# Kernel optimization log

Hardware: AMD Instinct MI355X
Metric: run time of the kernel (lower is better)

Reference implementation:

```python
import jax, jax.numpy as jnp
import numpy as np

N_NODES = 2048
N_EDGES = 16384
D_FEAT = 4  # 2*D_FEAT = 8 qubit angles per edge

# TTN circuit gate sequence: ('ry', wire, theta_idx) or ('cx', control, target)
OPS = [("ry",1,0),("ry",2,1),("cx",1,2),
       ("ry",5,2),("ry",6,3),("cx",6,5),
       ("ry",0,4),("ry",1,5),("cx",0,1),
       ("ry",2,6),("ry",3,7),("cx",3,2),
       ("ry",4,8),("ry",5,9),("cx",4,5),
       ("ry",6,10),("ry",7,11),("cx",7,6),
       ("ry",2,12),("ry",5,13),("cx",2,5),
       ("ry",1,14),("ry",2,15),("cx",1,2),
       ("ry",5,16),("ry",6,17),("cx",6,5),
       ("ry",2,18),("ry",5,19),("cx",2,5),
       ("ry",5,20)]

def setup_inputs() -> dict:
    key = jax.random.key(0)
    k1, k2, k3, k4 = jax.random.split(key, 4)
    X = jax.random.normal(k1, (N_NODES, D_FEAT), dtype=jnp.float32)
    Ri = jax.random.normal(k2, (N_NODES, N_EDGES), dtype=jnp.float32)
    Ro = jax.random.normal(k3, (N_NODES, N_EDGES), dtype=jnp.float32)
    theta = jax.random.uniform(k4, (21,), dtype=jnp.float32) * (4.0 * np.pi)
    return {"X": X, "Ri": Ri, "Ro": Ro, "theta": theta}

def _ry(state, w, th):
    # state: [B, 2,2,2,2,2,2,2,2]; apply RY(th) on wire w (real rotation)
    c = jnp.cos(0.5 * th)
    s = jnp.sin(0.5 * th)
    a0 = jnp.take(state, 0, axis=w + 1)
    a1 = jnp.take(state, 1, axis=w + 1)
    return jnp.stack([c * a0 - s * a1, s * a0 + c * a1], axis=w + 1)

def _cnot(state, c, t):
    s0 = jnp.take(state, 0, axis=c + 1)  # control=0 branch: unchanged
    s1 = jnp.take(state, 1, axis=c + 1)  # control=1 branch: flip target
    t_ax = t + 1 if t < c else t  # axis shift after removing control axis
    s1 = jnp.flip(s1, axis=t_ax)
    return jnp.stack([s0, s1], axis=c + 1)

def _circuit(angles, theta):
    # angles: [B, 8] per-edge RY encoding angles; all gates real -> real statevector
    B = angles.shape[0]
    half = 0.5 * angles
    amps = jnp.stack([jnp.cos(half), jnp.sin(half)], axis=-1)  # [B, 8, 2], RY(a)|0>
    state = amps[:, 0, :]  # [B, 2]
    for q in range(1, 8):  # product state build-up -> [B, 2^8]
        state = state[..., None] * amps[:, q, :].reshape((B,) + (1,) * q + (2,))
    for op in OPS:
        if op[0] == "ry":
            state = _ry(state, op[1], theta[op[2]])
        else:
            state = _cnot(state, op[1], op[2])
    p = state * state  # probabilities (real amplitudes)
    m = jnp.sum(p, axis=(1, 2, 3, 4, 5, 7, 8))  # marginal over wire 5 -> [B, 2]
    ez = m[:, 0] - m[:, 1]  # <Z_5>
    return (1.0 - ez) / 2.0

def reference(X, Ri, Ro, theta):
    bo = jnp.einsum('ne,nd->ed', Ro, X)  # [E, 4]
    bi = jnp.einsum('ne,nd->ed', Ri, X)  # [E, 4]
    angles = jnp.concatenate([bo, bi], axis=1)  # [E, 8]
    return _circuit(angles, theta)
```

## Files before the change

### kernel.cpp

```cpp
#include <hip/hip_runtime.h>
#include <cstdint>

constexpr int N_NODES  = 2048;
constexpr int N_EDGES  = 16384;
constexpr int NS       = 16;
constexpr int CHUNK    = N_NODES / NS;
constexpr int KSUB     = 4;
constexpr int SUBCHUNK = CHUNK / KSUB;
constexpr int TG       = 64;
constexpr int EPT      = 4;
constexpr int K1_BLOCK = 256;
constexpr int GROUPS   = N_EDGES / EPT;

__global__ __launch_bounds__(K1_BLOCK, 4) void k1_partial(
    const float* __restrict__ X,
    const float* __restrict__ Ri,
    const float* __restrict__ Ro,
    float* __restrict__ part)
{
    __shared__ float4 xs[CHUNK];
    const int ns  = blockIdx.y;
    const int n0  = ns * CHUNK;
    const int tid = threadIdx.x;
    if (tid < CHUNK) xs[tid] = reinterpret_cast<const float4*>(X)[n0 + tid];
    __syncthreads();

    const int lane = tid & 63;
    const int wv   = tid >> 6;
    const int gl   = lane & 15;
    const int ks   = lane >> 4;
    const int g    = blockIdx.x * TG + wv * 16 + gl;

    const float4* Ro4 = reinterpret_cast<const float4*>(Ro);
    const float4* Ri4 = reinterpret_cast<const float4*>(Ri);

    float acc_o[EPT][4];
    float acc_i[EPT][4];
    #pragma unroll
    for (int el = 0; el < EPT; ++el)
        #pragma unroll
        for (int q = 0; q < 4; ++q) { acc_o[el][q] = 0.f; acc_i[el][q] = 0.f; }

    const int kbase = ks * SUBCHUNK;
    #pragma unroll 8
    for (int k = 0; k < SUBCHUNK; ++k) {
        const int kk = kbase + k;
        const int n  = n0 + kk;
        const float4 ro = Ro4[(size_t)n * (N_EDGES / 4) + g];
        const float4 ri = Ri4[(size_t)n * (N_EDGES / 4) + g];
        const float4 x  = xs[kk];
        const float roa[EPT] = {ro.x, ro.y, ro.z, ro.w};
        const float ria[EPT] = {ri.x, ri.y, ri.z, ri.w};
        const float xa[4]    = {x.x,  x.y,  x.z,  x.w};
        #pragma unroll
        for (int el = 0; el < EPT; ++el)
            #pragma unroll
            for (int q = 0; q < 4; ++q) {
                acc_o[el][q] = fmaf(roa[el], xa[q], acc_o[el][q]);
                acc_i[el][q] = fmaf(ria[el], xa[q], acc_i[el][q]);
            }
    }

    float sum[32];
    #pragma unroll
    for (int q = 0; q < 4; ++q)
        #pragma unroll
        for (int el = 0; el < EPT; ++el) {
            sum[q * 4 + el]      = acc_o[el][q];
            sum[16 + q * 4 + el] = acc_i[el][q];
        }
    #pragma unroll
    for (int v = 0; v < 32; ++v) {
        sum[v] += __shfl_xor(sum[v], 16, 64);
        sum[v] += __shfl_xor(sum[v], 32, 64);
    }

    if (ks == 0) {
        #pragma unroll
        for (int el = 0; el < EPT; ++el) {
            const int e = 4 * g + el;
            float4* dst = reinterpret_cast<float4*>(part + ((size_t)ns * N_EDGES + e) * 8);
            dst[0] = make_float4(sum[0 + el], sum[4 + el], sum[8 + el], sum[12 + el]);
            dst[1] = make_float4(sum[16 + el], sum[20 + el], sum[24 + el], sum[28 + el]);
        }
    }
}

template<int LVL>
__device__ __forceinline__ void build64(float* st, float c, float s) {
    #pragma unroll
    for (int i = (1 << LVL) - 1; i >= 0; --i) {
        const float v = st[i];
        st[2 * i]     = v * c;
        st[2 * i + 1] = v * s;
    }
}

template<int W>
__device__ __forceinline__ void ry64(float* st, float c, float s) {
    constexpr int STRIDE = 1 << (7 - W);
    #pragma unroll
    for (int base = 0; base < 64; base += 2 * STRIDE)
        #pragma unroll
        for (int j = 0; j < STRIDE; ++j) {
            const int i0 = base + j, i1 = i0 + STRIDE;
            const float a0 = st[i0], a1 = st[i1];
            st[i0] = fmaf(c, a0, -(s * a1));
            st[i1] = fmaf(s, a0,   c * a1);
        }
}

__device__ __forceinline__ void ry_cross(float* st, float c, float s, int mask, int mybit) {
    const float ss = mybit ? s : -s;
    #pragma unroll
    for (int j = 0; j < 64; ++j) {
        const float other = __shfl_xor(st[j], mask, 64);
        st[j] = fmaf(c, st[j], ss * other);
    }
}

template<int CB, int TB>
__device__ __forceinline__ void cx_reg(float* st) {
    #pragma unroll
    for (int i = 0; i < 64; ++i)
        if ((i & CB) && !(i & TB)) {
            const float t = st[i]; st[i] = st[i | TB]; st[i | TB] = t;
        }
}

__global__ __launch_bounds__(256, 2) void k2_circuit(
    const float* __restrict__ part,
    const float* __restrict__ theta,
    float* __restrict__ out)
{
    const int tid = threadIdx.x;
    const int sub = tid & 3;
    const int e   = blockIdx.x * 64 + (tid >> 2);
    const int p0  = (sub >> 1) & 1;
    const int p1  = sub & 1;

    float a[8] = {0.f, 0.f, 0.f, 0.f, 0.f, 0.f, 0.f, 0.f};
    #pragma unroll
    for (int r = 0; r < 4; ++r) {
        const int ns = sub * 4 + r;
        const float4* p4 = reinterpret_cast<const float4*>(
            part + ((size_t)ns * N_EDGES + e) * 8);
        const float4 lo = p4[0], hi = p4[1];
        a[0] += lo.x; a[1] += lo.y; a[2] += lo.z; a[3] += lo.w;
        a[4] += hi.x; a[5] += hi.y; a[6] += hi.z; a[7] += hi.w;
    }
    #pragma unroll
    for (int q = 0; q < 8; ++q) {
        a[q] += __shfl_xor(a[q], 1, 64);
        a[q] += __shfl_xor(a[q], 2, 64);
    }

    float st[64];
    {
        float c, s, f;
        sincosf(0.5f * a[0], &s, &c); f  = p0 ? s : c;
        sincosf(0.5f * a[1], &s, &c); f *= p1 ? s : c;
        st[0] = f;
        sincosf(0.5f * a[2], &s, &c); build64<0>(st, c, s);
        sincosf(0.5f * a[3], &s, &c); build64<1>(st, c, s);
        sincosf(0.5f * a[4], &s, &c); build64<2>(st, c, s);
        sincosf(0.5f * a[5], &s, &c); build64<3>(st, c, s);
        sincosf(0.5f * a[6], &s, &c); build64<4>(st, c, s);
        sincosf(0.5f * a[7], &s, &c); build64<5>(st, c, s);
    }

#define THC(IDX) float c_, s_; __sincosf(0.5f * theta[IDX], &s_, &c_)
#define RYL(W, IDX) { THC(IDX); ry64<W>(st, c_, s_); }
#define RY0(IDX)    { THC(IDX); ry_cross(st, c_, s_, 2, p0); }
#define RY1(IDX)    { THC(IDX); ry_cross(st, c_, s_, 1, p1); }

    RY1(0) RYL(2, 1)
    {
        #pragma unroll
        for (int j = 0; j < 32; ++j) {
            const float t0 = st[j], t1 = st[j + 32];
            st[j]      = p1 ? t1 : t0;
            st[j + 32] = p1 ? t0 : t1;
        }
    }
    RYL(5, 2) RYL(6, 3) cx_reg<2, 4>(st);
    RY0(4) RY1(5)
    {
        #pragma unroll
        for (int j = 0; j < 64; ++j) {
            const float other = __shfl_xor(st[j], 1, 64);
            st[j] = p0 ? other : st[j];
        }
    }
    RYL(2, 6) RYL(3, 7) cx_reg<16, 32>(st);
    RYL(4, 8) RYL(5, 9) cx_reg<8, 4>(st);
    RYL(6, 10) RYL(7, 11) cx_reg<1, 2>(st);
    RYL(2, 12) RYL(5, 13) cx_reg<32, 4>(st);
    RY1(14) RYL(2, 15)
    {
        #pragma unroll
        for (int j = 0; j < 32; ++j) {
            const float t0 = st[j], t1 = st[j + 32];
            st[j]      = p1 ? t1 : t0;
            st[j + 32] = p1 ? t0 : t1;
        }
    }
    RYL(5, 16) RYL(6, 17) cx_reg<2, 4>(st);
    RYL(2, 18) RYL(5, 19) cx_reg<32, 4>(st);
    RYL(5, 20)
#undef RYL
#undef RY0
#undef RY1
#undef THC

    float m0 = 0.f, m1 = 0.f;
    #pragma unroll
    for (int j = 0; j < 64; ++j) {
        if (j & 4) m1 = fmaf(st[j], st[j], m1);
        else       m0 = fmaf(st[j], st[j], m0);
    }
    float d = m1 - m0;
    d += __shfl_xor(d, 1, 64);
    d += __shfl_xor(d, 2, 64);
    if (sub == 0) out[e] = 0.5f * (1.0f + d);
}

extern "C" void kernel_launch(void* const* d_in, const int* in_sizes, int n_in,
                              void* d_out, int out_size, void* d_ws, size_t ws_size,
                              hipStream_t stream)
{
    const float* X     = (const float*)d_in[0];
    const float* Ri    = (const float*)d_in[1];
    const float* Ro    = (const float*)d_in[2];
    const float* theta = (const float*)d_in[3];
    float* part = (float*)d_ws;
    float* outp = (float*)d_out;

    dim3 g1(GROUPS / TG, NS);
    k1_partial<<<g1, dim3(K1_BLOCK), 0, stream>>>(X, Ri, Ro, part);
    k2_circuit<<<dim3(N_EDGES / 64), dim3(256), 0, stream>>>(part, theta, outp);
}
```

Baseline: 61.69 us.

## Fuse edge projection and circuit simulation into one kernel with LDS reduction

```diff
diff --git a/kernel.cpp b/kernel.cpp
--- a/kernel.cpp
+++ b/kernel.cpp
@@ -1,90 +1,16 @@
 #include <hip/hip_runtime.h>
 #include <cstdint>
 
-constexpr int N_NODES  = 2048;
-constexpr int N_EDGES  = 16384;
-constexpr int NS       = 16;
-constexpr int CHUNK    = N_NODES / NS;
-constexpr int KSUB     = 4;
-constexpr int SUBCHUNK = CHUNK / KSUB;
-constexpr int TG       = 64;
-constexpr int EPT      = 4;
-constexpr int K1_BLOCK = 256;
-constexpr int GROUPS   = N_EDGES / EPT;
-
-__global__ __launch_bounds__(K1_BLOCK, 4) void k1_partial(
-    const float* __restrict__ X,
-    const float* __restrict__ Ri,
-    const float* __restrict__ Ro,
-    float* __restrict__ part)
-{
-    __shared__ float4 xs[CHUNK];
-    const int ns  = blockIdx.y;
-    const int n0  = ns * CHUNK;
-    const int tid = threadIdx.x;
-    if (tid < CHUNK) xs[tid] = reinterpret_cast<const float4*>(X)[n0 + tid];
-    __syncthreads();
-
-    const int lane = tid & 63;
-    const int wv   = tid >> 6;
-    const int gl   = lane & 15;
-    const int ks   = lane >> 4;
-    const int g    = blockIdx.x * TG + wv * 16 + gl;
-
-    const float4* Ro4 = reinterpret_cast<const float4*>(Ro);
-    const float4* Ri4 = reinterpret_cast<const float4*>(Ri);
-
-    float acc_o[EPT][4];
-    float acc_i[EPT][4];
-    #pragma unroll
-    for (int el = 0; el < EPT; ++el)
-        #pragma unroll
-        for (int q = 0; q < 4; ++q) { acc_o[el][q] = 0.f; acc_i[el][q] = 0.f; }
-
-    const int kbase = ks * SUBCHUNK;
-    #pragma unroll 8
-    for (int k = 0; k < SUBCHUNK; ++k) {
-        const int kk = kbase + k;
-        const int n  = n0 + kk;
-        const float4 ro = Ro4[(size_t)n * (N_EDGES / 4) + g];
-        const float4 ri = Ri4[(size_t)n * (N_EDGES / 4) + g];
-        const float4 x  = xs[kk];
-        const float roa[EPT] = {ro.x, ro.y, ro.z, ro.w};
-        const float ria[EPT] = {ri.x, ri.y, ri.z, ri.w};
-        const float xa[4]    = {x.x,  x.y,  x.z,  x.w};
-        #pragma unroll
-        for (int el = 0; el < EPT; ++el)
-            #pragma unroll
-            for (int q = 0; q < 4; ++q) {
-                acc_o[el][q] = fmaf(roa[el], xa[q], acc_o[el][q]);
-                acc_i[el][q] = fmaf(ria[el], xa[q], acc_i[el][q]);
-            }
-    }
-
-    float sum[32];
-    #pragma unroll
-    for (int q = 0; q < 4; ++q)
-        #pragma unroll
-        for (int el = 0; el < EPT; ++el) {
-            sum[q * 4 + el]      = acc_o[el][q];
-            sum[16 + q * 4 + el] = acc_i[el][q];
-        }
-    #pragma unroll
-    for (int v = 0; v < 32; ++v) {
-        sum[v] += __shfl_xor(sum[v], 16, 64);
-        sum[v] += __shfl_xor(sum[v], 32, 64);
-    }
-
-    if (ks == 0) {
-        #pragma unroll
-        for (int el = 0; el < EPT; ++el) {
-            const int e = 4 * g + el;
-            float4* dst = reinterpret_cast<float4*>(part + ((size_t)ns * N_EDGES + e) * 8);
-            dst[0] = make_float4(sum[0 + el], sum[4 + el], sum[8 + el], sum[12 + el]);
-            dst[1] = make_float4(sum[16 + el], sum[20 + el], sum[24 + el], sum[28 + el]);
-        }
-    }
-}
+constexpr int N_NODES = 2048;
+constexpr int N_EDGES = 16384;
+constexpr int NGRP    = 16;
+constexpr int TILE_E  = NGRP * 4;
+constexpr int WAVES   = 16;
+constexpr int BLK     = WAVES * 64;
+constexpr int ROWS_W  = N_NODES / WAVES;
+constexpr int ROWS_T  = ROWS_W / 4;
+constexpr int NBLK    = N_EDGES / TILE_E;
+
 
 template<int LVL>
 __device__ __forceinline__ void build64(float* st, float c, float s) {
@@ -128,101 +54,166 @@
         }
 }
 
-__global__ __launch_bounds__(256, 2) void k2_circuit(
-    const float* __restrict__ part,
+__global__ __launch_bounds__(BLK, 4) void fused_edgenet(
+    const float* __restrict__ X,
+    const float* __restrict__ Ri,
+    const float* __restrict__ Ro,
     const float* __restrict__ theta,
     float* __restrict__ out)
 {
-    const int tid = threadIdx.x;
-    const int sub = tid & 3;
-    const int e   = blockIdx.x * 64 + (tid >> 2);
-    const int p0  = (sub >> 1) & 1;
-    const int p1  = sub & 1;
-
-    float a[8] = {0.f, 0.f, 0.f, 0.f, 0.f, 0.f, 0.f, 0.f};
-    #pragma unroll
-    for (int r = 0; r < 4; ++r) {
-        const int ns = sub * 4 + r;
-        const float4* p4 = reinterpret_cast<const float4*>(
-            part + ((size_t)ns * N_EDGES + e) * 8);
-        const float4 lo = p4[0], hi = p4[1];
-        a[0] += lo.x; a[1] += lo.y; a[2] += lo.z; a[3] += lo.w;
-        a[4] += hi.x; a[5] += hi.y; a[6] += hi.z; a[7] += hi.w;
-    }
-    #pragma unroll
-    for (int q = 0; q < 8; ++q) {
-        a[q] += __shfl_xor(a[q], 1, 64);
-        a[q] += __shfl_xor(a[q], 2, 64);
-    }
-
-    float st[64];
-    {
-        float c, s, f;
-        sincosf(0.5f * a[0], &s, &c); f  = p0 ? s : c;
-        sincosf(0.5f * a[1], &s, &c); f *= p1 ? s : c;
-        st[0] = f;
-        sincosf(0.5f * a[2], &s, &c); build64<0>(st, c, s);
-        sincosf(0.5f * a[3], &s, &c); build64<1>(st, c, s);
-        sincosf(0.5f * a[4], &s, &c); build64<2>(st, c, s);
-        sincosf(0.5f * a[5], &s, &c); build64<3>(st, c, s);
-        sincosf(0.5f * a[6], &s, &c); build64<4>(st, c, s);
-        sincosf(0.5f * a[7], &s, &c); build64<5>(st, c, s);
-    }
+    __shared__ float red[WAVES][NGRP][33];
+
+    const int tid  = threadIdx.x;
+    const int w    = tid >> 6;
+    const int lane = tid & 63;
+    const int gl   = lane & 15;
+    const int ks   = lane >> 4;
+    const int g    = blockIdx.x * NGRP + gl;
+
+    const float4* Ro4 = reinterpret_cast<const float4*>(Ro);
+    const float4* Ri4 = reinterpret_cast<const float4*>(Ri);
+    const float4* X4  = reinterpret_cast<const float4*>(X);
+
+    float acc_o[4][4];
+    float acc_i[4][4];
+    #pragma unroll
+    for (int el = 0; el < 4; ++el)
+        #pragma unroll
+        for (int q = 0; q < 4; ++q) { acc_o[el][q] = 0.f; acc_i[el][q] = 0.f; }
+
+    const int n0 = w * ROWS_W + ks * ROWS_T;
+    #pragma unroll 4
+    for (int k = 0; k < ROWS_T; ++k) {
+        const int n = n0 + k;
+        const float4 ro = Ro4[(size_t)n * (N_EDGES / 4) + g];
+        const float4 ri = Ri4[(size_t)n * (N_EDGES / 4) + g];
+        const float4 x  = X4[n];
+        const float roa[4] = {ro.x, ro.y, ro.z, ro.w};
+        const float ria[4] = {ri.x, ri.y, ri.z, ri.w};
+        const float xa[4]  = {x.x,  x.y,  x.z,  x.w};
+        #pragma unroll
+        for (int el = 0; el < 4; ++el)
+            #pragma unroll
+            for (int q = 0; q < 4; ++q) {
+                acc_o[el][q] = fmaf(roa[el], xa[q], acc_o[el][q]);
+                acc_i[el][q] = fmaf(ria[el], xa[q], acc_i[el][q]);
+            }
+    }
+
+    float sum[32];
+    #pragma unroll
+    for (int q = 0; q < 4; ++q)
+        #pragma unroll
+        for (int el = 0; el < 4; ++el) {
+            sum[q * 4 + el]      = acc_o[el][q];
+            sum[16 + q * 4 + el] = acc_i[el][q];
+        }
+    #pragma unroll
+    for (int v = 0; v < 32; ++v) {
+        sum[v] += __shfl_xor(sum[v], 16, 64);
+        sum[v] += __shfl_xor(sum[v], 32, 64);
+    }
+
+    if (ks == 0) {
+        #pragma unroll
+        for (int v = 0; v < 32; ++v) red[w][gl][v] = sum[v];
+    }
+    __syncthreads();
+
+    if (tid < 4 * TILE_E) {
+        const int sub   = tid & 3;
+        const int e_loc = tid >> 2;
+        const int g2    = e_loc >> 2;
+        const int el    = e_loc & 3;
+        const int e     = blockIdx.x * TILE_E + e_loc;
+        const int p0    = (sub >> 1) & 1;
+        const int p1    = sub & 1;
+
+        float a[8] = {0.f, 0.f, 0.f, 0.f, 0.f, 0.f, 0.f, 0.f};
+        #pragma unroll
+        for (int r = 0; r < 4; ++r) {
+            const int ww = sub * 4 + r;
+            #pragma unroll
+            for (int q = 0; q < 4; ++q) {
+                a[q]     += red[ww][g2][q * 4 + el];
+                a[4 + q] += red[ww][g2][16 + q * 4 + el];
+            }
+        }
+        #pragma unroll
+        for (int q = 0; q < 8; ++q) {
+            a[q] += __shfl_xor(a[q], 1, 64);
+            a[q] += __shfl_xor(a[q], 2, 64);
+        }
+
+        float st[64];
+        {
+            float c, s, f;
+            sincosf(0.5f * a[0], &s, &c); f  = p0 ? s : c;
+            sincosf(0.5f * a[1], &s, &c); f *= p1 ? s : c;
+            st[0] = f;
+            sincosf(0.5f * a[2], &s, &c); build64<0>(st, c, s);
+            sincosf(0.5f * a[3], &s, &c); build64<1>(st, c, s);
+            sincosf(0.5f * a[4], &s, &c); build64<2>(st, c, s);
+            sincosf(0.5f * a[5], &s, &c); build64<3>(st, c, s);
+            sincosf(0.5f * a[6], &s, &c); build64<4>(st, c, s);
+            sincosf(0.5f * a[7], &s, &c); build64<5>(st, c, s);
+        }
 
 #define THC(IDX) float c_, s_; __sincosf(0.5f * theta[IDX], &s_, &c_)
 #define RYL(W, IDX) { THC(IDX); ry64<W>(st, c_, s_); }
 #define RY0(IDX)    { THC(IDX); ry_cross(st, c_, s_, 2, p0); }
 #define RY1(IDX)    { THC(IDX); ry_cross(st, c_, s_, 1, p1); }
 
-    RY1(0) RYL(2, 1)
-    {
-        #pragma unroll
-        for (int j = 0; j < 32; ++j) {
-            const float t0 = st[j], t1 = st[j + 32];
-            st[j]      = p1 ? t1 : t0;
-            st[j + 32] = p1 ? t0 : t1;
-        }
-    }
-    RYL(5, 2) RYL(6, 3) cx_reg<2, 4>(st);
-    RY0(4) RY1(5)
-    {
-        #pragma unroll
-        for (int j = 0; j < 64; ++j) {
-            const float other = __shfl_xor(st[j], 1, 64);
-            st[j] = p0 ? other : st[j];
-        }
-    }
-    RYL(2, 6) RYL(3, 7) cx_reg<16, 32>(st);
-    RYL(4, 8) RYL(5, 9) cx_reg<8, 4>(st);
-    RYL(6, 10) RYL(7, 11) cx_reg<1, 2>(st);
-    RYL(2, 12) RYL(5, 13) cx_reg<32, 4>(st);
-    RY1(14) RYL(2, 15)
-    {
-        #pragma unroll
-        for (int j = 0; j < 32; ++j) {
-            const float t0 = st[j], t1 = st[j + 32];
-            st[j]      = p1 ? t1 : t0;
-            st[j + 32] = p1 ? t0 : t1;
-        }
-    }
-    RYL(5, 16) RYL(6, 17) cx_reg<2, 4>(st);
-    RYL(2, 18) RYL(5, 19) cx_reg<32, 4>(st);
-    RYL(5, 20)
+        RY1(0) RYL(2, 1)
+        {
+            #pragma unroll
+            for (int j = 0; j < 32; ++j) {
+                const float t0 = st[j], t1 = st[j + 32];
+                st[j]      = p1 ? t1 : t0;
+                st[j + 32] = p1 ? t0 : t1;
+            }
+        }
+        RYL(5, 2) RYL(6, 3) cx_reg<2, 4>(st);
+        RY0(4) RY1(5)
+        {
+            #pragma unroll
+            for (int j = 0; j < 64; ++j) {
+                const float other = __shfl_xor(st[j], 1, 64);
+                st[j] = p0 ? other : st[j];
+            }
+        }
+        RYL(2, 6) RYL(3, 7) cx_reg<16, 32>(st);
+        RYL(4, 8) RYL(5, 9) cx_reg<8, 4>(st);
+        RYL(6, 10) RYL(7, 11) cx_reg<1, 2>(st);
+        RYL(2, 12) RYL(5, 13) cx_reg<32, 4>(st);
+        RY1(14) RYL(2, 15)
+        {
+            #pragma unroll
+            for (int j = 0; j < 32; ++j) {
+                const float t0 = st[j], t1 = st[j + 32];
+                st[j]      = p1 ? t1 : t0;
+                st[j + 32] = p1 ? t0 : t1;
+            }
+        }
+        RYL(5, 16) RYL(6, 17) cx_reg<2, 4>(st);
+        RYL(2, 18) RYL(5, 19) cx_reg<32, 4>(st);
+        RYL(5, 20)
 #undef RYL
 #undef RY0
 #undef RY1
 #undef THC
 
-    float m0 = 0.f, m1 = 0.f;
-    #pragma unroll
-    for (int j = 0; j < 64; ++j) {
-        if (j & 4) m1 = fmaf(st[j], st[j], m1);
-        else       m0 = fmaf(st[j], st[j], m0);
-    }
-    float d = m1 - m0;
-    d += __shfl_xor(d, 1, 64);
-    d += __shfl_xor(d, 2, 64);
-    if (sub == 0) out[e] = 0.5f * (1.0f + d);
+        float m0 = 0.f, m1 = 0.f;
+        #pragma unroll
+        for (int j = 0; j < 64; ++j) {
+            if (j & 4) m1 = fmaf(st[j], st[j], m1);
+            else       m0 = fmaf(st[j], st[j], m0);
+        }
+        float d = m1 - m0;
+        d += __shfl_xor(d, 1, 64);
+        d += __shfl_xor(d, 2, 64);
+        if (sub == 0) out[e] = 0.5f * (1.0f + d);
+    }
 }
 
 extern "C" void kernel_launch(void* const* d_in, const int* in_sizes, int n_in,
@@ -233,10 +224,7 @@
     const float* Ri    = (const float*)d_in[1];
     const float* Ro    = (const float*)d_in[2];
     const float* theta = (const float*)d_in[3];
-    float* part = (float*)d_ws;
     float* outp = (float*)d_out;
 
-    dim3 g1(GROUPS / TG, NS);
-    k1_partial<<<g1, dim3(K1_BLOCK), 0, stream>>>(X, Ri, Ro, part);
-    k2_circuit<<<dim3(N_EDGES / 64), dim3(256), 0, stream>>>(part, theta, outp);
-}
+    fused_edgenet<<<dim3(NBLK), dim3(BLK), 0, stream>>>(X, Ri, Ro, theta, outp);
+}
```

Measured after the change: 57.70 us. -6.5%, faster.
